# Optimization experiments

Measured on AMD Instinct MI355X. Metric: run time of the kernel, lower is better.

The kernel has to match this reference:

```python
import jax, jax.numpy as jnp
import numpy as np

N = 100000   # nodes
E = 1600000  # edges
F = 128      # input features
H = 128      # hidden
L = 4        # num_layers (1 conv1 + 3 convs)
S = 10000    # subgraphs
G = 256      # graphs
C = 10       # classes
BN_EPS = 1e-5


def setup_inputs() -> dict:
    key = jax.random.key(0)
    ks = jax.random.split(key, 12)
    x = jax.random.normal(ks[0], (N, F), jnp.float32)
    edge_index = jax.random.randint(ks[1], (2, E), 0, N, jnp.int32)
    node_to_subgraph = jnp.sort(jax.random.randint(ks[2], (N,), 0, S, jnp.int32))
    subgraph_to_graph = jnp.sort(jax.random.randint(ks[3], (S,), 0, G, jnp.int32))
    sc = 1.0 / np.sqrt(H)
    # stacked per-layer GIN MLP params (torch Linear layout [out, in]); F == H so conv1 stacks too
    W1 = jax.random.uniform(ks[4], (L, H, F), jnp.float32, -sc, sc)
    b1 = jax.random.uniform(ks[5], (L, H), jnp.float32, -sc, sc)
    g1 = jnp.ones((L, H), jnp.float32)
    be1 = jnp.zeros((L, H), jnp.float32)
    W2 = jax.random.uniform(ks[6], (L, H, H), jnp.float32, -sc, sc)
    b2 = jax.random.uniform(ks[7], (L, H), jnp.float32, -sc, sc)
    g2 = jnp.ones((L, H), jnp.float32)
    be2 = jnp.zeros((L, H), jnp.float32)
    eps = jnp.zeros((L,), jnp.float32)  # train_eps=True, init 0
    sc1 = 1.0 / np.sqrt(L * H)
    lin1_W = jax.random.uniform(ks[8], (H, L * H), jnp.float32, -sc1, sc1)
    lin1_b = jax.random.uniform(ks[9], (H,), jnp.float32, -sc1, sc1)
    lin2_W = jax.random.uniform(ks[10], (C, H), jnp.float32, -sc, sc)
    lin2_b = jax.random.uniform(ks[11], (C,), jnp.float32, -sc, sc)
    return dict(x=x, edge_index=edge_index, node_to_subgraph=node_to_subgraph,
                subgraph_to_graph=subgraph_to_graph, W1=W1, b1=b1, g1=g1, be1=be1,
                W2=W2, b2=b2, g2=g2, be2=be2, eps=eps,
                lin1_W=lin1_W, lin1_b=lin1_b, lin2_W=lin2_W, lin2_b=lin2_b)


def _bn(h, g, b):
    mu = h.mean(axis=0)
    var = jnp.mean((h - mu) ** 2, axis=0)  # biased var (training-mode BN)
    return (h - mu) * jax.lax.rsqrt(var + BN_EPS) * g + b


def _seg_mean(f, seg, num_segments):
    s = jax.ops.segment_sum(f, seg, num_segments=num_segments)
    cnt = jax.ops.segment_sum(jnp.ones((f.shape[0], 1), f.dtype), seg, num_segments=num_segments)
    return s / jnp.maximum(cnt, 1.0)


def reference(x, edge_index, node_to_subgraph, subgraph_to_graph,
              W1, b1, g1, be1, W2, b2, g2, be2, eps,
              lin1_W, lin1_b, lin2_W, lin2_b):
    src, dst = edge_index[0], edge_index[1]

    def layer(xc, p):
        w1, bb1, gg1, bt1, w2, bb2, gg2, bt2, e = p
        agg = jax.ops.segment_sum(xc[src], dst, num_segments=N)  # neighbor sum
        h = (1.0 + e) * xc + agg
        h = jax.nn.relu(_bn(h @ w1.T + bb1, gg1, bt1))
        h = jax.nn.relu(_bn(h @ w2.T + bb2, gg2, bt2))
        return h, h

    _, ys = jax.lax.scan(layer, x, (W1, b1, g1, be1, W2, b2, g2, be2, eps))  # [L, N, H]
    feat = jnp.transpose(ys, (1, 0, 2)).reshape(N, L * H)  # torch.cat(xs, dim=1)
    sub = _seg_mean(feat, node_to_subgraph, S)   # [S, L*H]
    gph = _seg_mean(sub, subgraph_to_graph, G)   # [G, L*H]
    h = jax.nn.relu(gph @ lin1_W.T + lin1_b)
    out = h @ lin2_W.T + lin2_b                  # dropout inactive in eval
    return jax.nn.log_softmax(out, axis=-1)
```

## Files before the change

### kernel.cpp

```cpp
#include <hip/hip_runtime.h>

typedef unsigned int u32;
typedef unsigned short u16;

#define NN 100000
#define EE 1600000
#define SS 10000
#define GG 256
#define NSCAN ((NN + 1023) / 1024)

#define O_W1   0
#define O_B1   65536
#define O_G1   66048
#define O_BE1  66560
#define O_W2   67072
#define O_B2   132608
#define O_G2   133120
#define O_BE2  133632
#define O_EPS  134144
#define O_L1W  134148
#define O_L1B  199684
#define O_L2W  199812
#define O_L2B  201092
#define NPAR   201102

typedef __bf16 bf16x8_t __attribute__((ext_vector_type(8)));
typedef float f32x4_t __attribute__((ext_vector_type(4)));
typedef u32 u32x4_t __attribute__((ext_vector_type(4)));

__device__ __forceinline__ float bf2f(u16 u) {
  union { u32 i; float f; } x; x.i = ((u32)u) << 16; return x.f;
}
__device__ __forceinline__ u16 f2bf(float f) {
  union { float f; u32 i; } x; x.f = f;
  u32 r = x.i + 0x7fffu + ((x.i >> 16) & 1u);
  return (u16)(r >> 16);
}
__device__ __forceinline__ int lbound(const int* __restrict__ a, int n, int key) {
  int lo = 0, hi = n;
  while (lo < hi) { int mid = (lo + hi) >> 1; if (a[mid] < key) lo = mid + 1; else hi = mid; }
  return lo;
}

__global__ void k_sniff(const u16* __restrict__ x, int* __restrict__ flag) {
  __shared__ int cnt;
  if (threadIdx.x == 0) cnt = 0;
  __syncthreads();
  int weird = 0;
  for (int i = threadIdx.x; i < 8192; i += 256) {
    u16 v = x[i];
    int e = (v >> 7) & 0xff;
    if (e >= 0xC0) weird++;
  }
  atomicAdd(&cnt, weird);
  __syncthreads();
  if (threadIdx.x == 0) *flag = (cnt > 64) ? 1 : 0;
}

__global__ __launch_bounds__(256) void k_cvt_params(
    const void* pW1, const void* pb1, const void* pg1, const void* pbe1,
    const void* pW2, const void* pb2, const void* pg2, const void* pbe2,
    const void* peps, const void* pl1w, const void* pl1b, const void* pl2w, const void* pl2b,
    const int* __restrict__ flagp, float* __restrict__ P) {
  int i = blockIdx.x * 256 + threadIdx.x;
  if (i >= NPAR) return;
  const void* src; int rel;
  if      (i < O_B1)  { src = pW1;  rel = i - O_W1; }
  else if (i < O_G1)  { src = pb1;  rel = i - O_B1; }
  else if (i < O_BE1) { src = pg1;  rel = i - O_G1; }
  else if (i < O_W2)  { src = pbe1; rel = i - O_BE1; }
  else if (i < O_B2)  { src = pW2;  rel = i - O_W2; }
  else if (i < O_G2)  { src = pb2;  rel = i - O_B2; }
  else if (i < O_BE2) { src = pg2;  rel = i - O_G2; }
  else if (i < O_EPS) { src = pbe2; rel = i - O_BE2; }
  else if (i < O_L1W) { src = peps; rel = i - O_EPS; }
  else if (i < O_L1B) { src = pl1w; rel = i - O_L1W; }
  else if (i < O_L2W) { src = pl1b; rel = i - O_L1B; }
  else if (i < O_L2B) { src = pl2w; rel = i - O_L2W; }
  else                { src = pl2b; rel = i - O_L2B; }
  float v = (*flagp) ? ((const float*)src)[rel] : bf2f(((const u16*)src)[rel]);
  P[i] = v;
}

__global__ __launch_bounds__(256) void k_cvtW(const float* __restrict__ P,
                                              u16* __restrict__ W1b, u16* __restrict__ W2b) {
  int i = blockIdx.x * 256 + threadIdx.x;
  if (i >= 131072) return;
  if (i < 65536) W1b[i] = f2bf(P[O_W1 + i]);
  else           W2b[i - 65536] = f2bf(P[O_W2 + i - 65536]);
}

__global__ __launch_bounds__(256) void k_prep(const void* __restrict__ x, const int* __restrict__ flagp,
                                              u16* __restrict__ Z0) {
  int i = blockIdx.x * 256 + threadIdx.x;
  if (i >= (NN * 128) / 8) return;
  if (*flagp) {
    const float4* xf = (const float4*)x;
    float4 a = xf[i * 2], b = xf[i * 2 + 1];
    u32x4_t o;
    o[0] = (u32)f2bf(a.x) | ((u32)f2bf(a.y) << 16);
    o[1] = (u32)f2bf(a.z) | ((u32)f2bf(a.w) << 16);
    o[2] = (u32)f2bf(b.x) | ((u32)f2bf(b.y) << 16);
    o[3] = (u32)f2bf(b.z) | ((u32)f2bf(b.w) << 16);
    *(u32x4_t*)(Z0 + i * 8) = o;
  } else {
    *(u32x4_t*)(Z0 + i * 8) = ((const u32x4_t*)x)[i];
  }
}

__global__ __launch_bounds__(256) void k_hist(const int* __restrict__ dst, int* __restrict__ cnt) {
  int i = blockIdx.x * 256 + threadIdx.x;
  if (i < EE) atomicAdd(&cnt[dst[i]], 1);
}

__global__ __launch_bounds__(256) void k_scan1(const int* __restrict__ cnt, int* __restrict__ bsum) {
  __shared__ int sh[256];
  int base = blockIdx.x * 1024 + threadIdx.x * 4;
  int s = 0;
#pragma unroll
  for (int i = 0; i < 4; i++) { int idx = base + i; s += (idx < NN) ? cnt[idx] : 0; }
  sh[threadIdx.x] = s; __syncthreads();
  for (int o = 128; o > 0; o >>= 1) {
    if (threadIdx.x < o) sh[threadIdx.x] += sh[threadIdx.x + o];
    __syncthreads();
  }
  if (threadIdx.x == 0) bsum[blockIdx.x] = sh[0];
}

__global__ void k_scan2(int* __restrict__ bsum, int* __restrict__ off) {
  if (threadIdx.x == 0 && blockIdx.x == 0) {
    int run = 0;
    for (int i = 0; i < NSCAN; i++) { int v = bsum[i]; bsum[i] = run; run += v; }
    off[NN] = run;
  }
}

__global__ __launch_bounds__(256) void k_scan3(const int* __restrict__ cnt, const int* __restrict__ bsum,
                                               int* __restrict__ off) {
  __shared__ int sh[256];
  int base = blockIdx.x * 1024 + threadIdx.x * 4;
  int v[4]; int s = 0;
#pragma unroll
  for (int i = 0; i < 4; i++) { int idx = base + i; v[i] = (idx < NN) ? cnt[idx] : 0; s += v[i]; }
  sh[threadIdx.x] = s; __syncthreads();
  for (int o = 1; o < 256; o <<= 1) {
    int add = (threadIdx.x >= o) ? sh[threadIdx.x - o] : 0;
    __syncthreads();
    sh[threadIdx.x] += add;
    __syncthreads();
  }
  int run = sh[threadIdx.x] - s + bsum[blockIdx.x];
#pragma unroll
  for (int i = 0; i < 4; i++) { int idx = base + i; if (idx < NN) { off[idx] = run; run += v[i]; } }
}

__global__ __launch_bounds__(256) void k_fill(const int* __restrict__ src, const int* __restrict__ dst,
                                              const int* __restrict__ off, int* __restrict__ cur,
                                              int* __restrict__ csr) {
  int i = blockIdx.x * 256 + threadIdx.x;
  if (i >= EE) return;
  int d = dst[i];
  int p = off[d] + atomicAdd(&cur[d], 1);
  csr[p] = src[i];
}

template <int MODE>
__global__ __launch_bounds__(256) void k_agg_gemm(
    const u16* __restrict__ Z, const int* __restrict__ off, const int* __restrict__ csr,
    const u16* __restrict__ Wb, const float* __restrict__ bias, const float* __restrict__ P,
    int layer, const float* __restrict__ st_prev, const float* __restrict__ gw,
    const float* __restrict__ bw, u16* __restrict__ H, float* __restrict__ st) {
  __shared__ __align__(16) u16 lds[4][16][136];
  __shared__ __align__(16) int shidx[4][512];
  int wave = threadIdx.x >> 6, lane = threadIdx.x & 63;
  int r0 = blockIdx.x * 64 + wave * 16;
  float ev = 1.0f + P[O_EPS + layer];
  int slot = lane >> 4;
  int cb = (lane & 15) * 8;

  float scl[8], shf[8];
  if (MODE) {
#pragma unroll
    for (int k = 0; k < 8; k++) {
      int c = cb + k;
      float mu = st_prev[c] * (1.0f / NN);
      float var = fmaxf(st_prev[128 + c] * (1.0f / NN) - mu * mu, 0.f);
      float s = gw[c] * rsqrtf(var + 1e-5f);
      scl[k] = s; shf[k] = bw[c] - mu * s;
    }
  }

  int offv = 0;
  if (lane <= 16) {
    int rr = r0 + lane; if (rr > NN) rr = NN; if (rr < 0) rr = 0;
    offv = off[rr];
  }
  int ebase = __shfl(offv, 0, 64);
  int eend  = __shfl(offv, 16, 64);
  int tn = eend - ebase;
  int nst = tn < 512 ? tn : 512;
  for (int i = lane; i < nst; i += 64) shidx[wave][i] = csr[ebase + i];

  for (int rr = 0; rr < 16; rr++) {
    int row = r0 + rr;
    float acc[8];
#pragma unroll
    for (int k = 0; k < 8; k++) acc[k] = 0.f;
    if (row < NN) {
      int s = __shfl(offv, rr, 64), e = __shfl(offv, rr + 1, 64);
      int n = e - s, b = s - ebase;
      int m = n + 1;
      auto nbr = [&](int j) -> int {
        int t = b + j - 1;
        return (t < 512) ? shidx[wave][t] : csr[ebase + t];
      };
      auto consume = [&](u32x4_t d, float c) {
#pragma unroll
        for (int k = 0; k < 4; k++) {
          float v0 = bf2f((u16)(d[k] & 0xffffu));
          float v1 = bf2f((u16)(d[k] >> 16));
          if (MODE) {
            v0 = fmaxf(fmaf(v0, scl[2 * k], shf[2 * k]), 0.f);
            v1 = fmaxf(fmaf(v1, scl[2 * k + 1], shf[2 * k + 1]), 0.f);
          }
          acc[2 * k]     = fmaf(v0, c, acc[2 * k]);
          acc[2 * k + 1] = fmaf(v1, c, acc[2 * k + 1]);
        }
      };
      int g = 0;
      for (; g + 16 <= m; g += 16) {
        int j0 = g + slot;
        int i0 = (j0 == 0) ? row : nbr(j0);
        int i1 = nbr(j0 + 4), i2 = nbr(j0 + 8), i3 = nbr(j0 + 12);
        u32x4_t d0 = *(const u32x4_t*)(Z + (size_t)i0 * 128 + cb);
        u32x4_t d1 = *(const u32x4_t*)(Z + (size_t)i1 * 128 + cb);
        u32x4_t d2 = *(const u32x4_t*)(Z + (size_t)i2 * 128 + cb);
        u32x4_t d3 = *(const u32x4_t*)(Z + (size_t)i3 * 128 + cb);
        consume(d0, (j0 == 0) ? ev : 1.f);
        consume(d1, 1.f); consume(d2, 1.f); consume(d3, 1.f);
      }
      for (; g < m; g += 4) {
        int j = g + slot;
        int idx = row; float c = 0.f;
        if (j < m) { c = 1.f; if (j > 0) idx = nbr(j); else c = ev; }
        u32x4_t d = *(const u32x4_t*)(Z + (size_t)idx * 128 + cb);
        consume(d, c);
      }
#pragma unroll
      for (int k = 0; k < 8; k++) {
        acc[k] += __shfl_xor(acc[k], 16, 64);
        acc[k] += __shfl_xor(acc[k], 32, 64);
      }
    }
    if (lane < 16) {
      u32x4_t o;
#pragma unroll
      for (int k = 0; k < 4; k++)
        o[k] = (u32)f2bf(acc[2 * k]) | ((u32)f2bf(acc[2 * k + 1]) << 16);
      *(u32x4_t*)&lds[wave][rr][cb] = o;
    }
  }

  int nidx = lane & 15, q = lane >> 4;
  f32x4_t acc[8];
  f32x4_t z4 = {0.f, 0.f, 0.f, 0.f};
#pragma unroll
  for (int ot = 0; ot < 8; ot++) acc[ot] = z4;
#pragma unroll
  for (int ks = 0; ks < 4; ks++) {
    bf16x8_t af = __builtin_bit_cast(bf16x8_t, *(const u32x4_t*)&lds[wave][nidx][ks * 32 + q * 8]);
#pragma unroll
    for (int ot = 0; ot < 8; ot++) {
      bf16x8_t bfr = __builtin_bit_cast(bf16x8_t, *(const u32x4_t*)(Wb + (ot * 16 + nidx) * 128 + ks * 32 + q * 8));
      acc[ot] = __builtin_amdgcn_mfma_f32_16x16x32_bf16(af, bfr, acc[ot], 0, 0, 0);
    }
  }
  float* sstw = (float*)&shidx[wave][0];
#pragma unroll
  for (int ot = 0; ot < 8; ot++) {
    int col = ot * 16 + nidx;
    float bv = bias[col];
    float s = 0.f, sq = 0.f;
#pragma unroll
    for (int j = 0; j < 4; j++) {
      int row = r0 + q * 4 + j;
      if (row < NN) {
        float v = acc[ot][j] + bv;
        u16 h = f2bf(v);
        float vr = bf2f(h);
        H[row * 128 + col] = h;
        s += vr; sq += vr * vr;
      }
    }
    s  += __shfl_xor(s, 16, 64);  s  += __shfl_xor(s, 32, 64);
    sq += __shfl_xor(sq, 16, 64); sq += __shfl_xor(sq, 32, 64);
    if (q == 0) { sstw[col] = s; sstw[128 + col] = sq; }
  }
  __syncthreads();
  int t = threadIdx.x;
  float tot = ((float*)&shidx[0][0])[t] + ((float*)&shidx[1][0])[t] +
              ((float*)&shidx[2][0])[t] + ((float*)&shidx[3][0])[t];
  atomicAdd(&st[t], tot);
}

__global__ __launch_bounds__(256) void k_bn_gemm(
    const u16* __restrict__ Hin, const u16* __restrict__ Wb, const float* __restrict__ bias,
    const float* __restrict__ st_in, const float* __restrict__ gw, const float* __restrict__ bw,
    u16* __restrict__ Hout, float* __restrict__ st_out) {
  __shared__ float sc[256];
  __shared__ float sst[4][256];
  int t = threadIdx.x;
  if (t < 128) {
    float mu = st_in[t] * (1.0f / NN);
    float var = st_in[128 + t] * (1.0f / NN) - mu * mu;
    var = fmaxf(var, 0.f);
    float r = rsqrtf(var + 1e-5f);
    float scl = gw[t] * r;
    sc[t] = scl;
    sc[128 + t] = bw[t] - mu * scl;
  }
  __syncthreads();
  int wave = t >> 6, lane = t & 63;
  int r0 = blockIdx.x * 64 + wave * 16;
  int nidx = lane & 15, q = lane >> 4;
  int arow = r0 + nidx;
  u32x4_t zero4 = {0, 0, 0, 0};
  u32x4_t raw[4];
#pragma unroll
  for (int ks = 0; ks < 4; ks++)
    raw[ks] = (arow < NN) ? *(const u32x4_t*)(Hin + arow * 128 + ks * 32 + q * 8) : zero4;
  f32x4_t acc[8];
  f32x4_t z4 = {0.f, 0.f, 0.f, 0.f};
#pragma unroll
  for (int ot = 0; ot < 8; ot++) acc[ot] = z4;
#pragma unroll
  for (int ks = 0; ks < 4; ks++) {
    int k0 = ks * 32 + q * 8;
    u32x4_t ap;
#pragma unroll
    for (int w = 0; w < 4; w++) {
      int k = k0 + 2 * w;
      float v0 = fmaxf(bf2f((u16)(raw[ks][w] & 0xffffu)) * sc[k] + sc[128 + k], 0.f);
      float v1 = fmaxf(bf2f((u16)(raw[ks][w] >> 16)) * sc[k + 1] + sc[128 + k + 1], 0.f);
      ap[w] = (u32)f2bf(v0) | ((u32)f2bf(v1) << 16);
    }
    bf16x8_t af = __builtin_bit_cast(bf16x8_t, ap);
#pragma unroll
    for (int ot = 0; ot < 8; ot++) {
      bf16x8_t bfr = __builtin_bit_cast(bf16x8_t, *(const u32x4_t*)(Wb + (ot * 16 + nidx) * 128 + k0));
      acc[ot] = __builtin_amdgcn_mfma_f32_16x16x32_bf16(af, bfr, acc[ot], 0, 0, 0);
    }
  }
#pragma unroll
  for (int ot = 0; ot < 8; ot++) {
    int col = ot * 16 + nidx;
    float bv = bias[col];
    float s = 0.f, sq = 0.f;
#pragma unroll
    for (int j = 0; j < 4; j++) {
      int row = r0 + q * 4 + j;
      if (row < NN) {
        float v = acc[ot][j] + bv;
        u16 h = f2bf(v);
        float vr = bf2f(h);
        Hout[row * 128 + col] = h;
        s += vr; sq += vr * vr;
      }
    }
    s  += __shfl_xor(s, 16, 64);  s  += __shfl_xor(s, 32, 64);
    sq += __shfl_xor(sq, 16, 64); sq += __shfl_xor(sq, 32, 64);
    if (q == 0) { sst[wave][col] = s; sst[wave][128 + col] = sq; }
  }
  __syncthreads();
  float tot = sst[0][t] + sst[1][t] + sst[2][t] + sst[3][t];
  atomicAdd(&st_out[t], tot);
}

__global__ __launch_bounds__(256) void k_sub(
    const u16* __restrict__ Hin, const float* __restrict__ st_in, const float* __restrict__ gw,
    const float* __restrict__ bw, const int* __restrict__ n2s,
    float* __restrict__ sub, int layer) {
  __shared__ float sc[256];
  int t = threadIdx.x;
  if (t < 128) {
    float mu = st_in[t] * (1.0f / NN);
    float var = st_in[128 + t] * (1.0f / NN) - mu * mu;
    var = fmaxf(var, 0.f);
    float r = rsqrtf(var + 1e-5f);
    float scl = gw[t] * r;
    sc[t] = scl;
    sc[128 + t] = bw[t] - mu * scl;
  }
  __syncthreads();
  int s = (blockIdx.x * 256 + t) >> 6;
  int lane = t & 63;
  if (s >= SS) return;
  int r0 = lbound(n2s, NN, s), r1 = lbound(n2s, NN, s + 1);
  float scl0 = sc[2 * lane], scl1 = sc[2 * lane + 1];
  float sh0 = sc[128 + 2 * lane], sh1 = sc[128 + 2 * lane + 1];
  const u32* hr = (const u32*)Hin;
  float a0 = 0.f, a1 = 0.f;
  for (int r = r0; r < r1; r++) {
    u32 d = hr[r * 64 + lane];
    a0 += fmaxf(bf2f((u16)(d & 0xffffu)) * scl0 + sh0, 0.f);
    a1 += fmaxf(bf2f((u16)(d >> 16)) * scl1 + sh1, 0.f);
  }
  int c = r1 - r0;
  float inv = 1.0f / (float)(c > 0 ? c : 1);
  float2 v; v.x = a0 * inv; v.y = a1 * inv;
  *(float2*)(sub + (size_t)s * 512 + layer * 128 + lane * 2) = v;
}

__global__ __launch_bounds__(256) void k_graphpool(const float* __restrict__ sub, const int* __restrict__ s2g,
                                                   float* __restrict__ gph) {
  int g = (blockIdx.x * 256 + threadIdx.x) >> 6;
  int lane = threadIdx.x & 63;
  if (g >= GG) return;
  int r0 = lbound(s2g, SS, g), r1 = lbound(s2g, SS, g + 1);
  float a[8] = {0.f, 0.f, 0.f, 0.f, 0.f, 0.f, 0.f, 0.f};
  for (int s = r0; s < r1; s++) {
    const float* row = sub + (size_t)s * 512 + lane * 8;
#pragma unroll
    for (int j = 0; j < 8; j++) a[j] += row[j];
  }
  int c = r1 - r0;
  float inv = 1.0f / (float)(c > 0 ? c : 1);
  float* orow = gph + (size_t)g * 512 + lane * 8;
#pragma unroll
  for (int j = 0; j < 8; j++) orow[j] = a[j] * inv;
}

__global__ __launch_bounds__(128) void k_head(const float* __restrict__ gph, const float* __restrict__ P,
                                              const int* __restrict__ flagp, void* __restrict__ out) {
  __shared__ float gsh[512];
  __shared__ float hsh[128];
  __shared__ float lsh[12];
  int g = blockIdx.x, t = threadIdx.x;
  for (int i = t; i < 512; i += 128) gsh[i] = gph[(size_t)g * 512 + i];
  __syncthreads();
  float acc = P[O_L1B + t];
  const float4* wr = (const float4*)(P + O_L1W + t * 512);
  for (int kb = 0; kb < 128; kb++) {
    float4 w = wr[kb];
    int k = kb * 4;
    acc += gsh[k] * w.x + gsh[k + 1] * w.y + gsh[k + 2] * w.z + gsh[k + 3] * w.w;
  }
  hsh[t] = fmaxf(acc, 0.f);
  __syncthreads();
  if (t < 10) {
    float a = P[O_L2B + t];
    const float* w2r = P + O_L2W + t * 128;
    for (int k = 0; k < 128; k++) a += hsh[k] * w2r[k];
    lsh[t] = a;
  }
  __syncthreads();
  if (t == 0) {
    float m = -1e30f;
    for (int c = 0; c < 10; c++) m = fmaxf(m, lsh[c]);
    float se = 0.f;
    for (int c = 0; c < 10; c++) se += expf(lsh[c] - m);
    lsh[10] = m + logf(se);
  }
  __syncthreads();
  if (t < 10) {
    float v = lsh[t] - lsh[10];
    if (*flagp) ((float*)out)[g * 10 + t] = v;
    else        ((u16*)out)[g * 10 + t] = f2bf(v);
  }
}

extern "C" void kernel_launch(void* const* d_in, const int* in_sizes, int n_in,
                              void* d_out, int out_size, void* d_ws, size_t ws_size,
                              hipStream_t stream) {
  const void* x   = d_in[0];
  const int* ei   = (const int*)d_in[1];
  const int* n2s  = (const int*)d_in[2];
  const int* s2g  = (const int*)d_in[3];

  char* ws = (char*)d_ws;
  size_t o = 0;
  auto alloc = [&](size_t b) -> void* {
    void* p = ws + o;
    o += (b + 255) & ~(size_t)255;
    return p;
  };
  int* flag    = (int*)alloc(256);
  int* off     = (int*)alloc((NN + 1) * 4);
  int* cnt     = (int*)alloc(NN * 4);
  int* bsum    = (int*)alloc(NSCAN * 4);
  int* csr     = (int*)alloc((size_t)EE * 4);
  u16* Z0      = (u16*)alloc((size_t)NN * 128 * 2);
  u16* H1      = (u16*)alloc((size_t)NN * 128 * 2);
  u16* H2A     = (u16*)alloc((size_t)NN * 128 * 2);
  u16* H2B     = (u16*)alloc((size_t)NN * 128 * 2);
  float* sub   = (float*)alloc((size_t)SS * 512 * 4);
  float* gph   = (float*)alloc((size_t)GG * 512 * 4);
  float* stats = (float*)alloc(8 * 256 * 4);
  float* P     = (float*)alloc((size_t)NPAR * 4);
  u16* W1b     = (u16*)alloc(65536 * 2);
  u16* W2b     = (u16*)alloc(65536 * 2);

  const int* esrc = ei;
  const int* edst = ei + EE;

  hipMemsetAsync(cnt, 0, NN * 4, stream);
  hipMemsetAsync(stats, 0, 8 * 256 * 4, stream);

  k_sniff<<<dim3(1), dim3(256), 0, stream>>>((const u16*)x, flag);
  k_cvt_params<<<dim3((NPAR + 255) / 256), dim3(256), 0, stream>>>(
      d_in[4], d_in[5], d_in[6], d_in[7], d_in[8], d_in[9], d_in[10], d_in[11],
      d_in[12], d_in[13], d_in[14], d_in[15], d_in[16], flag, P);
  k_cvtW<<<dim3(512), dim3(256), 0, stream>>>(P, W1b, W2b);
  k_prep<<<dim3((NN * 128 / 8 + 255) / 256), dim3(256), 0, stream>>>(x, flag, Z0);

  k_hist<<<dim3((EE + 255) / 256), dim3(256), 0, stream>>>(edst, cnt);
  k_scan1<<<dim3(NSCAN), dim3(256), 0, stream>>>(cnt, bsum);
  k_scan2<<<dim3(1), dim3(64), 0, stream>>>(bsum, off);
  k_scan3<<<dim3(NSCAN), dim3(256), 0, stream>>>(cnt, bsum, off);
  hipMemsetAsync(cnt, 0, NN * 4, stream);
  k_fill<<<dim3((EE + 255) / 256), dim3(256), 0, stream>>>(esrc, edst, off, cnt, csr);

  const u16* H2prev = Z0;
  for (int l = 0; l < 4; l++) {
    u16* H2cur = (l & 1) ? H2B : H2A;
    float* st1 = stats + (2 * l) * 256;
    float* st2 = stats + (2 * l + 1) * 256;
    if (l == 0) {
      k_agg_gemm<0><<<dim3((NN + 63) / 64), dim3(256), 0, stream>>>(
          H2prev, off, csr, W1b, P + O_B1, P, 0, P, P, P, H1, st1);
    } else {
      k_agg_gemm<1><<<dim3((NN + 63) / 64), dim3(256), 0, stream>>>(
          H2prev, off, csr, W1b + l * 16384, P + O_B1 + l * 128, P, l,
          stats + (2 * l - 1) * 256, P + O_G2 + (l - 1) * 128, P + O_BE2 + (l - 1) * 128, H1, st1);
    }
    k_bn_gemm<<<dim3((NN + 63) / 64), dim3(256), 0, stream>>>(
        H1, W2b + l * 16384, P + O_B2 + l * 128, st1, P + O_G1 + l * 128, P + O_BE1 + l * 128, H2cur, st2);
    k_sub<<<dim3((SS + 3) / 4), dim3(256), 0, stream>>>(
        H2cur, st2, P + O_G2 + l * 128, P + O_BE2 + l * 128, n2s, sub, l);
    H2prev = H2cur;
  }
  k_graphpool<<<dim3((GG + 3) / 4), dim3(256), 0, stream>>>(sub, s2g, gph);
  k_head<<<dim3(GG), dim3(128), 0, stream>>>(gph, P, flag, (void*)d_out);
}
```

Before: 1.274 ms.

## Gather each neighbor row across the whole wave instead of four 16-lane slots

The neighbor aggregation in the fused aggregate-GEMM kernel now has each of the 64 lanes load one 32-bit word (two bf16 channels) of every neighbor row. It unrolls eight neighbor loads at a time. This replaces the previous scheme where four 16-lane slots each fetched 16-byte chunks of different neighbors and then reduced across slots with shuffles. The change drops the cross-lane reduction and the per-lane 8-channel BN scale/shift registers, and lowers register pressure. In exchange each memory instruction moves less data per lane, so more load instructions are issued per edge, and row-level parallelism across neighbors drops to the unroll depth.

```diff
diff --git a/kernel.cpp b/kernel.cpp
--- a/kernel.cpp
+++ b/kernel.cpp
@@ -175,19 +175,19 @@
   int wave = threadIdx.x >> 6, lane = threadIdx.x & 63;
   int r0 = blockIdx.x * 64 + wave * 16;
   float ev = 1.0f + P[O_EPS + layer];
-  int slot = lane >> 4;
-  int cb = (lane & 15) * 8;
-
-  float scl[8], shf[8];
+  const u32* zr = (const u32*)Z;
+
+  float scl0 = 1.f, scl1 = 1.f, sh0 = 0.f, sh1 = 0.f;
   if (MODE) {
-#pragma unroll
-    for (int k = 0; k < 8; k++) {
-      int c = cb + k;
-      float mu = st_prev[c] * (1.0f / NN);
-      float var = fmaxf(st_prev[128 + c] * (1.0f / NN) - mu * mu, 0.f);
-      float s = gw[c] * rsqrtf(var + 1e-5f);
-      scl[k] = s; shf[k] = bw[c] - mu * s;
-    }
+    int cc0 = 2 * lane, cc1 = 2 * lane + 1;
+    float mu0 = st_prev[cc0] * (1.0f / NN);
+    float v0 = fmaxf(st_prev[128 + cc0] * (1.0f / NN) - mu0 * mu0, 0.f);
+    scl0 = gw[cc0] * rsqrtf(v0 + 1e-5f);
+    sh0 = bw[cc0] - mu0 * scl0;
+    float mu1 = st_prev[cc1] * (1.0f / NN);
+    float v1 = fmaxf(st_prev[128 + cc1] * (1.0f / NN) - mu1 * mu1, 0.f);
+    scl1 = gw[cc1] * rsqrtf(v1 + 1e-5f);
+    sh1 = bw[cc1] - mu1 * scl1;
   }
 
   int offv = 0;
@@ -201,64 +201,51 @@
   int nst = tn < 512 ? tn : 512;
   for (int i = lane; i < nst; i += 64) shidx[wave][i] = csr[ebase + i];
 
+  auto cvt0 = [&](u32 d) -> float {
+    float v = bf2f((u16)(d & 0xffffu));
+    if (MODE) v = fmaxf(fmaf(v, scl0, sh0), 0.f);
+    return v;
+  };
+  auto cvt1 = [&](u32 d) -> float {
+    float v = bf2f((u16)(d >> 16));
+    if (MODE) v = fmaxf(fmaf(v, scl1, sh1), 0.f);
+    return v;
+  };
+
   for (int rr = 0; rr < 16; rr++) {
     int row = r0 + rr;
-    float acc[8];
-#pragma unroll
-    for (int k = 0; k < 8; k++) acc[k] = 0.f;
+    float a0 = 0.f, a1 = 0.f;
     if (row < NN) {
       int s = __shfl(offv, rr, 64), e = __shfl(offv, rr + 1, 64);
       int n = e - s, b = s - ebase;
-      int m = n + 1;
-      auto nbr = [&](int j) -> int {
-        int t = b + j - 1;
-        return (t < 512) ? shidx[wave][t] : csr[ebase + t];
-      };
-      auto consume = [&](u32x4_t d, float c) {
-#pragma unroll
-        for (int k = 0; k < 4; k++) {
-          float v0 = bf2f((u16)(d[k] & 0xffffu));
-          float v1 = bf2f((u16)(d[k] >> 16));
-          if (MODE) {
-            v0 = fmaxf(fmaf(v0, scl[2 * k], shf[2 * k]), 0.f);
-            v1 = fmaxf(fmaf(v1, scl[2 * k + 1], shf[2 * k + 1]), 0.f);
-          }
-          acc[2 * k]     = fmaf(v0, c, acc[2 * k]);
-          acc[2 * k + 1] = fmaf(v1, c, acc[2 * k + 1]);
+      u32 d = zr[row * 64 + lane];
+      a0 = ev * cvt0(d);
+      a1 = ev * cvt1(d);
+      const int* ip = (b + n <= 512) ? &shidx[wave][b] : &csr[s];
+      int i = 0;
+      for (; i + 7 < n; i += 8) {
+        u32 dd[8];
+#pragma unroll
+        for (int j = 0; j < 8; j++) dd[j] = zr[ip[i + j] * 64 + lane];
+#pragma unroll
+        for (int j = 0; j < 8; j++) {
+          a0 += cvt0(dd[j]);
+          a1 += cvt1(dd[j]);
         }
-      };
-      int g = 0;
-      for (; g + 16 <= m; g += 16) {
-        int j0 = g + slot;
-        int i0 = (j0 == 0) ? row : nbr(j0);
-        int i1 = nbr(j0 + 4), i2 = nbr(j0 + 8), i3 = nbr(j0 + 12);
-        u32x4_t d0 = *(const u32x4_t*)(Z + (size_t)i0 * 128 + cb);
-        u32x4_t d1 = *(const u32x4_t*)(Z + (size_t)i1 * 128 + cb);
-        u32x4_t d2 = *(const u32x4_t*)(Z + (size_t)i2 * 128 + cb);
-        u32x4_t d3 = *(const u32x4_t*)(Z + (size_t)i3 * 128 + cb);
-        consume(d0, (j0 == 0) ? ev : 1.f);
-        consume(d1, 1.f); consume(d2, 1.f); consume(d3, 1.f);
       }
-      for (; g < m; g += 4) {
-        int j = g + slot;
-        int idx = row; float c = 0.f;
-        if (j < m) { c = 1.f; if (j > 0) idx = nbr(j); else c = ev; }
-        u32x4_t d = *(const u32x4_t*)(Z + (size_t)idx * 128 + cb);
-        consume(d, c);
+      for (; i + 1 < n; i += 2) {
+        u32 d0 = zr[ip[i] * 64 + lane];
+        u32 d1 = zr[ip[i + 1] * 64 + lane];
+        a0 += cvt0(d0) + cvt0(d1);
+        a1 += cvt1(d0) + cvt1(d1);
       }
-#pragma unroll
-      for (int k = 0; k < 8; k++) {
-        acc[k] += __shfl_xor(acc[k], 16, 64);
-        acc[k] += __shfl_xor(acc[k], 32, 64);
+      if (i < n) {
+        u32 d0 = zr[ip[i] * 64 + lane];
+        a0 += cvt0(d0);
+        a1 += cvt1(d0);
       }
     }
-    if (lane < 16) {
-      u32x4_t o;
-#pragma unroll
-      for (int k = 0; k < 4; k++)
-        o[k] = (u32)f2bf(acc[2 * k]) | ((u32)f2bf(acc[2 * k + 1]) << 16);
-      *(u32x4_t*)&lds[wave][rr][cb] = o;
-    }
+    ((u32*)&lds[wave][rr][0])[lane] = (u32)f2bf(a0) | ((u32)f2bf(a1) << 16);
   }
 
   int nidx = lane & 15, q = lane >> 4;
```

Result: faster. 1.219 ms (-4.3%).
